# Performance work log

Hardware: AMD Instinct MI355X
Metric: run time of the kernel (lower is better)

## Reference

```python
import jax, jax.numpy as jnp
import numpy as np

LEAKY_SLOPE = 0.2  # tf.nn.leaky_relu default alpha
L2_EPS = 1e-12     # tf.nn.l2_normalize default epsilon


def setup_inputs() -> dict:
    key = jax.random.key(0)
    N, d, E, k = 100000, 64, 1600000, 3
    k0, k1, k2, k3 = jax.random.split(key, 4)
    x = jax.random.normal(k0, (N, d), dtype=jnp.float32)
    edge_index = jax.random.randint(k1, (2, E), 0, N, dtype=jnp.int32)
    scale = 1.0 / np.sqrt(d).astype(np.float32)
    W_gcn = jax.random.normal(k2, (k, d, d), dtype=jnp.float32) * scale
    W_int = jax.random.normal(k3, (k, d, d), dtype=jnp.float32) * scale
    b_gcn = jnp.zeros((k, d), dtype=jnp.float32)
    b_int = jnp.zeros((k, d), dtype=jnp.float32)
    return {"x": x, "edge_index": edge_index, "W_gcn": W_gcn, "b_gcn": b_gcn,
            "W_int": W_int, "b_int": b_int}


def _l2norm(h):
    sq = jnp.sum(h * h, axis=-1, keepdims=True)
    return h * jax.lax.rsqrt(jnp.maximum(sq, L2_EPS))


def reference(x, edge_index, W_gcn, b_gcn, W_int, b_int):
    N = x.shape[0]
    row, col = edge_index[0], edge_index[1]
    # LightGCN.norm_adj: symmetric normalization D^-1/2 A D^-1/2 (no self-loops)
    deg = jax.ops.segment_sum(jnp.ones_like(row, dtype=x.dtype), row, num_segments=N)
    dinv = jnp.where(deg > 0, jax.lax.rsqrt(deg), 0.0)
    w = dinv[row] * dinv[col]  # [E]

    def agg(h):
        # sparse normed_adj @ h : gather source feats, scale, scatter-add to dst
        return jax.ops.segment_sum(w[:, None] * h[col], row, num_segments=N)

    lrelu = lambda z: jax.nn.leaky_relu(z, LEAKY_SLOPE)
    h = x
    outs = [x]
    for i in range(W_gcn.shape[0]):
        ha = agg(h)  # [N, d]
        h = lrelu(ha @ W_gcn[i] + b_gcn[i]) + lrelu((h * ha) @ W_int[i] + b_int[i])
        outs.append(_l2norm(h))
    return jnp.concatenate(outs, axis=-1)  # [N, (k+1)*d]
```

## Files before the change

kernel.cpp:

```cpp
#include <hip/hip_runtime.h>


#define LEAKY 0.2f
#define NBK_MAX 512
#define TILE_A 4096
#define BCAP 5120

typedef unsigned short ushort_t;
typedef unsigned char uchar_t;
typedef short short8 __attribute__((ext_vector_type(8)));
typedef float f32x4 __attribute__((ext_vector_type(4)));
typedef float f32x2 __attribute__((ext_vector_type(2)));

__device__ __forceinline__ float lrelu(float z) { return z > 0.f ? z : LEAKY * z; }

__device__ __forceinline__ unsigned f2bf(float f) {
  unsigned u = __float_as_uint(f);
  return (u + 0x7FFFu + ((u >> 16) & 1u)) >> 16;
}

__device__ __forceinline__ float bf2f(unsigned u) {
  return __uint_as_float(u << 16);
}

__device__ __forceinline__ unsigned f2fp8(float f) {
  return (unsigned)__builtin_amdgcn_cvt_pk_fp8_f32(f, f, 0, false) & 0xFFu;
}

__device__ __forceinline__ int rfl(const int* p) {
  return __builtin_amdgcn_readfirstlane(*p);
}

__global__ __launch_bounds__(256) void bucket_k(const int* __restrict__ row,
                                                const int* __restrict__ col,
                                                int* __restrict__ tails,
                                                unsigned int* __restrict__ buckets,
                                                int E, int nbk) {
  __shared__ int bcnt[NBK_MAX], bex[NBK_MAX], bnext[NBK_MAX], gbase[NBK_MAX];
  __shared__ int ssc[256];
  int t = threadIdx.x;
  int ts = blockIdx.x * TILE_A;
  int tn = E - ts;
  if (tn > TILE_A) tn = TILE_A;
  bcnt[t] = 0;
  bcnt[t + 256] = 0;
  __syncthreads();
  for (int i = t; i < tn; i += 256) atomicAdd(&bcnt[row[ts + i] >> 8], 1);
  __syncthreads();
  int a0 = bcnt[2 * t], a1 = bcnt[2 * t + 1];
  ssc[t] = a0 + a1;
  __syncthreads();
  #pragma unroll
  for (int off = 1; off < 256; off <<= 1) {
    int x = (t >= off) ? ssc[t - off] : 0;
    __syncthreads();
    ssc[t] += x;
    __syncthreads();
  }
  int ex = ssc[t] - (a0 + a1);
  bex[2 * t] = ex;
  bex[2 * t + 1] = ex + a0;
  bnext[2 * t] = ex;
  bnext[2 * t + 1] = ex + a0;
  if (t < nbk && bcnt[t] > 0) gbase[t] = atomicAdd(&tails[t], bcnt[t]);
  int t2 = t + 256;
  if (t2 < nbk && bcnt[t2] > 0) gbase[t2] = atomicAdd(&tails[t2], bcnt[t2]);
  __syncthreads();
  for (int i = t; i < tn; i += 256) {
    int r = row[ts + i], c = col[ts + i];
    int b = r >> 8;
    int k = atomicAdd(&bnext[b], 1) - bex[b];
    int pos = gbase[b] + k;
    if (pos < BCAP)
      buckets[(size_t)b * BCAP + pos] = ((unsigned)(r & 255) << 24) | (unsigned)c;
  }
}

__global__ __launch_bounds__(512) void bkscan_k(const int* __restrict__ tails,
                                                int* __restrict__ bkbase,
                                                int* __restrict__ rp,
                                                int nbk, int N, int E) {
  __shared__ int s[512];
  int t = threadIdx.x;
  int v = (t < nbk) ? tails[t] : 0;
  s[t] = v;
  __syncthreads();
  #pragma unroll
  for (int off = 1; off < 512; off <<= 1) {
    int x = (t >= off) ? s[t - off] : 0;
    __syncthreads();
    s[t] += x;
    __syncthreads();
  }
  if (t < nbk) bkbase[t] = s[t] - v;
  if (t == 0) rp[N] = E;
}

__global__ __launch_bounds__(256) void csr_k(const int* __restrict__ tails,
                                             const int* __restrict__ bkbase,
                                             const unsigned int* __restrict__ buckets,
                                             int* __restrict__ rp,
                                             float* __restrict__ dinv,
                                             int* __restrict__ packed, int N) {
  __shared__ int cnt[256], sc[256], cnt2[256];
  int b = blockIdx.x, t = threadIdx.x;
  int row0 = b << 8;
  int nrows = N - row0;
  if (nrows > 256) nrows = 256;
  int cb = tails[b];
  if (cb > BCAP) cb = BCAP;
  int base = bkbase[b];
  const unsigned int* ent = buckets + (size_t)b * BCAP;
  cnt[t] = 0;
  __syncthreads();
  for (int i = t; i < cb; i += 256) atomicAdd(&cnt[ent[i] >> 24], 1);
  __syncthreads();
  int v = cnt[t];
  sc[t] = v;
  __syncthreads();
  #pragma unroll
  for (int off = 1; off < 256; off <<= 1) {
    int x = (t >= off) ? sc[t - off] : 0;
    __syncthreads();
    sc[t] += x;
    __syncthreads();
  }
  int ex = sc[t] - v;
  if (t < nrows) {
    rp[row0 + t] = base + ex;
    dinv[row0 + t] = (v > 0) ? rsqrtf((float)v) : 0.f;
  }
  cnt[t] = ex;
  cnt2[t] = 0;
  __syncthreads();
  for (int i = t; i < cb; i += 256) {
    unsigned e = ent[i];
    int rl = e >> 24;
    int slot = atomicAdd(&cnt2[rl], 1);
    packed[base + cnt[rl] + slot] = (int)(e & 0xFFFFFFu);
  }
}

__global__ __launch_bounds__(256) void copyx_k(const float* __restrict__ x,
                                               const float* __restrict__ dinv,
                                               float* __restrict__ out,
                                               ushort_t* __restrict__ xb,
                                               uchar_t* __restrict__ xg,
                                               int N, int ostride4) {
  int total = N * 16;
  int stride = gridDim.x * blockDim.x;
  for (int i = blockIdx.x * blockDim.x + threadIdx.x; i < total; i += stride) {
    int n = i >> 4, c4 = i & 15;
    float4 v = ((const float4*)x)[i];
    ((float4*)out)[(size_t)n * ostride4 + c4] = v;
    unsigned p0 = f2bf(v.x) | (f2bf(v.y) << 16);
    unsigned p1 = f2bf(v.z) | (f2bf(v.w) << 16);
    ((uint2*)xb)[i] = make_uint2(p0, p1);
    float dv = dinv[n];
    unsigned pkA =
        (unsigned)__builtin_amdgcn_cvt_pk_fp8_f32(v.x * dv, v.y * dv, 0, false);
    unsigned pkB =
        (unsigned)__builtin_amdgcn_cvt_pk_fp8_f32(v.z * dv, v.w * dv, 0, false);
    ((unsigned*)xg)[i] = (pkA & 0xFFFFu) | ((pkB & 0xFFFFu) << 16);
  }
}

__global__ __launch_bounds__(256) void packw_k(const float* __restrict__ Wg,
                                               const float* __restrict__ Wi,
                                               ushort_t* __restrict__ Wfrag,
                                               int total,
                                               int* __restrict__ tails, int nbk) {
  int tid = blockIdx.x * 256 + threadIdx.x;
  if (tid < nbk) tails[tid] = 0;
  if (tid >= total) return;
  int lane = tid & 63;
  int kh = (tid >> 6) & 1;
  int nt = (tid >> 7) & 3;
  int gm = (tid >> 9) & 1;
  int ly = tid >> 10;
  const float* W = (gm ? Wi : Wg) + (size_t)ly * 4096;
  int kb = (kh << 5) + ((lane >> 4) << 3);
  int n = (nt << 4) + (lane & 15);
  unsigned u[4];
  #pragma unroll
  for (int j = 0; j < 4; ++j) {
    unsigned lo = f2bf(W[(kb + 2 * j) * 64 + n]);
    unsigned hi = f2bf(W[(kb + 2 * j + 1) * 64 + n]);
    u[j] = lo | (hi << 16);
  }
  ((uint4*)Wfrag)[tid] = make_uint4(u[0], u[1], u[2], u[3]);
}

__global__ __launch_bounds__(256) void agg_k(const int* __restrict__ rp,
                                             const int* __restrict__ packed,
                                             const float* __restrict__ dinv,
                                             const uchar_t* __restrict__ gin,
                                             ushort_t* __restrict__ ha, int N) {
  int wv = (((blockIdx.x << 2) + (threadIdx.x >> 6)) << 1);
  if (wv >= N) return;
  int lane = threadIdx.x & 63;
  int grp = lane >> 3;
  int l8 = lane & 7;
  bool have1 = (wv + 1) < N;
  int s0 = rfl(&rp[wv]);
  int e0 = rfl(&rp[wv + 1]);
  int s1 = have1 ? rfl(&rp[wv + 1]) : 0;
  int e1 = have1 ? rfl(&rp[wv + 2]) : 0;
  float dr0 = __int_as_float(__builtin_amdgcn_readfirstlane(__float_as_int(dinv[wv])));
  float dr1 = have1 ? __int_as_float(__builtin_amdgcn_readfirstlane(
                          __float_as_int(dinv[wv + 1])))
                    : 0.f;
  float a0[8], a1[8];
  #pragma unroll
  for (int i = 0; i < 8; ++i) { a0[i] = 0.f; a1[i] = 0.f; }
  int bidx0 = grp << 2;
  int ch0 = s0, ch1 = s1;
  while (ch0 < e0 || ch1 < e1) {
    int m0 = e0 - ch0;
    if (m0 > 64) m0 = 64;
    int m1 = e1 - ch1;
    if (m1 > 64) m1 = 64;
    int cl0 = (m0 > 0 && lane < m0) ? packed[ch0 + lane] : 0;
    int cl1 = (m1 > 0 && lane < m1) ? packed[ch1 + lane] : 0;
    int mm = m0 > m1 ? m0 : m1;
    int nit = (mm + 7) >> 3;
    #pragma unroll 2
    for (int j = 0; j < nit; ++j) {
      int bi = bidx0 + (j << 5);
      int c0 = __builtin_amdgcn_ds_bpermute(bi, cl0);
      int c1 = __builtin_amdgcn_ds_bpermute(bi, cl1);
      int eidx = (j << 3) + grp;
      float msk0 = (eidx < m0) ? 1.f : 0.f;
      float msk1 = (eidx < m1) ? 1.f : 0.f;
      uint2 v0 = ((const uint2*)(gin + ((size_t)c0 << 6)))[l8];
      uint2 v1 = ((const uint2*)(gin + ((size_t)c1 << 6)))[l8];
      f32x2 d;
      d = __builtin_amdgcn_cvt_pk_f32_fp8((int)v0.x, false);
      a0[0] = fmaf(msk0, d[0], a0[0]);  a0[1] = fmaf(msk0, d[1], a0[1]);
      d = __builtin_amdgcn_cvt_pk_f32_fp8((int)v0.x, true);
      a0[2] = fmaf(msk0, d[0], a0[2]);  a0[3] = fmaf(msk0, d[1], a0[3]);
      d = __builtin_amdgcn_cvt_pk_f32_fp8((int)v0.y, false);
      a0[4] = fmaf(msk0, d[0], a0[4]);  a0[5] = fmaf(msk0, d[1], a0[5]);
      d = __builtin_amdgcn_cvt_pk_f32_fp8((int)v0.y, true);
      a0[6] = fmaf(msk0, d[0], a0[6]);  a0[7] = fmaf(msk0, d[1], a0[7]);
      d = __builtin_amdgcn_cvt_pk_f32_fp8((int)v1.x, false);
      a1[0] = fmaf(msk1, d[0], a1[0]);  a1[1] = fmaf(msk1, d[1], a1[1]);
      d = __builtin_amdgcn_cvt_pk_f32_fp8((int)v1.x, true);
      a1[2] = fmaf(msk1, d[0], a1[2]);  a1[3] = fmaf(msk1, d[1], a1[3]);
      d = __builtin_amdgcn_cvt_pk_f32_fp8((int)v1.y, false);
      a1[4] = fmaf(msk1, d[0], a1[4]);  a1[5] = fmaf(msk1, d[1], a1[5]);
      d = __builtin_amdgcn_cvt_pk_f32_fp8((int)v1.y, true);
      a1[6] = fmaf(msk1, d[0], a1[6]);  a1[7] = fmaf(msk1, d[1], a1[7]);
    }
    ch0 += 64;
    ch1 += 64;
  }
  #pragma unroll
  for (int off = 8; off < 64; off <<= 1)
    #pragma unroll
    for (int i = 0; i < 8; ++i) {
      a0[i] += __shfl_xor(a0[i], off);
      a1[i] += __shfl_xor(a1[i], off);
    }
  if (grp == 0) {
    unsigned u0 = f2bf(a0[0] * dr0) | (f2bf(a0[1] * dr0) << 16);
    unsigned u1 = f2bf(a0[2] * dr0) | (f2bf(a0[3] * dr0) << 16);
    unsigned u2 = f2bf(a0[4] * dr0) | (f2bf(a0[5] * dr0) << 16);
    unsigned u3 = f2bf(a0[6] * dr0) | (f2bf(a0[7] * dr0) << 16);
    ((uint4*)(ha + ((size_t)wv << 6)))[l8] = make_uint4(u0, u1, u2, u3);
  } else if (grp == 1 && have1) {
    unsigned u0 = f2bf(a1[0] * dr1) | (f2bf(a1[1] * dr1) << 16);
    unsigned u1 = f2bf(a1[2] * dr1) | (f2bf(a1[3] * dr1) << 16);
    unsigned u2 = f2bf(a1[4] * dr1) | (f2bf(a1[5] * dr1) << 16);
    unsigned u3 = f2bf(a1[6] * dr1) | (f2bf(a1[7] * dr1) << 16);
    ((uint4*)(ha + ((size_t)(wv + 1) << 6)))[l8] = make_uint4(u0, u1, u2, u3);
  }
}

__global__ __launch_bounds__(256) void gemmM_k(const ushort_t* __restrict__ ha,
                                               const ushort_t* __restrict__ hin,
                                               const ushort_t* __restrict__ Wfrag,
                                               const float* __restrict__ bg,
                                               const float* __restrict__ bi,
                                               const float* __restrict__ dinv,
                                               ushort_t* __restrict__ hout,
                                               uchar_t* __restrict__ gout,
                                               float* __restrict__ outp,
                                               int N, int ntiles, int ostride,
                                               int writeg) {
  int lane = threadIdx.x & 63;
  int gq = lane >> 4, ln15 = lane & 15;
  const short8* wf = (const short8*)Wfrag;
  short8 bG[8], bI[8];
  #pragma unroll
  for (int nt = 0; nt < 4; ++nt)
    #pragma unroll
    for (int kh = 0; kh < 2; ++kh) {
      bG[nt * 2 + kh] = wf[nt * 128 + kh * 64 + lane];
      bI[nt * 2 + kh] = wf[512 + nt * 128 + kh * 64 + lane];
    }
  float bgv[4], biv[4];
  #pragma unroll
  for (int nt = 0; nt < 4; ++nt) {
    bgv[nt] = bg[nt * 16 + ln15];
    biv[nt] = bi[nt * 16 + ln15];
  }
  int wid = (blockIdx.x << 2) + (threadIdx.x >> 6);
  int nw = gridDim.x << 2;
  for (int tile = wid; tile < ntiles; tile += nw) {
    int node0 = tile << 4;
    const short8* pa =
        (const short8*)(ha + (size_t)(node0 + ln15) * 64 + gq * 8);
    const short8* ph =
        (const short8*)(hin + (size_t)(node0 + ln15) * 64 + gq * 8);
    f32x4 acc1[4], acc2[4];
    #pragma unroll
    for (int nt = 0; nt < 4; ++nt) {
      acc1[nt] = (f32x4){bgv[nt], bgv[nt], bgv[nt], bgv[nt]};
      acc2[nt] = (f32x4){biv[nt], biv[nt], biv[nt], biv[nt]};
    }
    #pragma unroll
    for (int kh = 0; kh < 2; ++kh) {
      short8 af = pa[kh * 4];
      short8 hf = ph[kh * 4];
      short8 vmf;
      #pragma unroll
      for (int e2 = 0; e2 < 8; ++e2) {
        float fa = bf2f((ushort_t)af[e2]);
        float fh = bf2f((ushort_t)hf[e2]);
        vmf[e2] = (short)f2bf(fa * fh);
      }
      #pragma unroll
      for (int nt = 0; nt < 4; ++nt) {
        acc1[nt] = __builtin_amdgcn_mfma_f32_16x16x32_bf16(af, bG[nt * 2 + kh],
                                                           acc1[nt], 0, 0, 0);
        acc2[nt] = __builtin_amdgcn_mfma_f32_16x16x32_bf16(vmf, bI[nt * 2 + kh],
                                                           acc2[nt], 0, 0, 0);
      }
    }
    float z[4][4];
    float ssr[4] = {0.f, 0.f, 0.f, 0.f};
    #pragma unroll
    for (int nt = 0; nt < 4; ++nt)
      #pragma unroll
      for (int reg = 0; reg < 4; ++reg) {
        float zz = lrelu(acc1[nt][reg]) + lrelu(acc2[nt][reg]);
        z[nt][reg] = zz;
        ssr[reg] = fmaf(zz, zz, ssr[reg]);
      }
    #pragma unroll
    for (int off = 1; off < 16; off <<= 1)
      #pragma unroll
      for (int reg = 0; reg < 4; ++reg) ssr[reg] += __shfl_xor(ssr[reg], off);
    float inv[4];
    #pragma unroll
    for (int reg = 0; reg < 4; ++reg)
      inv[reg] = rsqrtf(fmaxf(ssr[reg], 1e-12f));
    #pragma unroll
    for (int reg = 0; reg < 4; ++reg) {
      int r = node0 + 4 * gq + reg;
      if (r < N) {
        float dv = dinv[r];
        #pragma unroll
        for (int nt = 0; nt < 4; ++nt) {
          outp[(size_t)r * ostride + nt * 16 + ln15] = z[nt][reg] * inv[reg];
          hout[(size_t)r * 64 + nt * 16 + ln15] = (ushort_t)f2bf(z[nt][reg]);
          if (writeg)
            gout[(size_t)r * 64 + nt * 16 + ln15] =
                (uchar_t)f2fp8(z[nt][reg] * dv);
        }
      }
    }
  }
}

extern "C" void kernel_launch(void* const* d_in, const int* in_sizes, int n_in,
                              void* d_out, int out_size, void* d_ws, size_t ws_size,
                              hipStream_t stream) {
  const float* x  = (const float*)d_in[0];
  const int*   ei = (const int*)d_in[1];
  const float* Wg = (const float*)d_in[2];
  const float* bg = (const float*)d_in[3];
  const float* Wi = (const float*)d_in[4];
  const float* bi = (const float*)d_in[5];
  float* out = (float*)d_out;

  const int d = 64;
  const int N = in_sizes[0] / d;
  const int E = in_sizes[1] / 2;
  const int K = in_sizes[2] / (d * d);
  const int* row = ei;
  const int* col = ei + E;
  const int nbk = (N + 255) / 256;
  const int N16 = (N + 15) & ~15;
  const int ntiles = N16 / 16;
  const int ostride = (K + 1) * d;

  char* ws = (char*)d_ws;
  size_t off = 0;
  auto alloc = [&](size_t bytes) {
    char* p = ws + off;
    off = (off + bytes + 255) & ~(size_t)255;
    return p;
  };
  int*   tails  = (int*)alloc((size_t)NBK_MAX * 4);
  int*   bkbase = (int*)alloc((size_t)NBK_MAX * 4);
  int*   rp     = (int*)alloc((size_t)(N + 1) * 4);
  float* dinv   = (float*)alloc((size_t)N16 * 4);
  unsigned int* buckets = (unsigned int*)alloc((size_t)nbk * BCAP * 4);
  int*   packed = (int*)alloc((size_t)E * 4);
  ushort_t* ha  = (ushort_t*)alloc((size_t)N16 * d * 2);
  ushort_t* hb0 = (ushort_t*)alloc((size_t)N16 * d * 2);
  ushort_t* hb1 = (ushort_t*)alloc((size_t)N16 * d * 2);
  ushort_t* xb  = (ushort_t*)alloc((size_t)N16 * d * 2);
  uchar_t* hg0  = (uchar_t*)alloc((size_t)N16 * d);
  uchar_t* hg1  = (uchar_t*)alloc((size_t)N16 * d);
  uchar_t* xg   = (uchar_t*)alloc((size_t)N16 * d);
  ushort_t* Wfrag = (ushort_t*)alloc((size_t)K * 8192 * 2);
  (void)ws_size;

  int wtotal = K * 1024;
  packw_k<<<(wtotal + 255) / 256, 256, 0, stream>>>(Wg, Wi, Wfrag, wtotal,
                                                    tails, nbk);
  int ntA = (E + TILE_A - 1) / TILE_A;
  bucket_k<<<ntA, 256, 0, stream>>>(row, col, tails, buckets, E, nbk);
  bkscan_k<<<1, 512, 0, stream>>>(tails, bkbase, rp, nbk, N, E);
  csr_k<<<nbk, 256, 0, stream>>>(tails, bkbase, buckets, rp, dinv, packed, N);
  copyx_k<<<2048, 256, 0, stream>>>(x, dinv, out, xb, xg, N, ostride / 4);

  const ushort_t* hin = xb;
  const uchar_t* gin = xg;
  ushort_t* hbufs[2] = {hb0, hb1};
  uchar_t* gbufs[2] = {hg0, hg1};
  int aggblocks = (N + 7) / 8;
  for (int i = 0; i < K; ++i) {
    ushort_t* hout = hbufs[i & 1];
    uchar_t* gout = gbufs[i & 1];
    agg_k<<<aggblocks, 256, 0, stream>>>(rp, packed, dinv, gin, ha, N);
    gemmM_k<<<1024, 256, 0, stream>>>(
        ha, hin, Wfrag + (size_t)i * 8192, bg + (size_t)i * d,
        bi + (size_t)i * d, dinv, hout, gout, out + (size_t)(i + 1) * d,
        N, ntiles, ostride, (i + 1 < K) ? 1 : 0);
    hin = hout;
    gin = gout;
  }
}
```

Measured before the change: 223.7 us.

## Fuse CSR preprocessing kernels and aggregate four rows per wavefront

The bucket-scan kernel is folded into bucket_k through a last-block-done atomic counter, and the x copy/convert kernel is folded into csr_k using per-block shared dinv. This removes two launches and a dependent global dinv read. agg_k now handles four destination rows per wavefront instead of two, giving more independent gathers in flight at the cost of extra registers. The last layer's gemm also skips writing the bf16 and fp8 hidden buffers it never reads. The last-block pattern depends on atomics for memory visibility.

New measurement: 236.5 us. 5.8% more time.

```diff
diff --git a/kernel.cpp b/kernel.cpp
--- a/kernel.cpp
+++ b/kernel.cpp
@@ -31,138 +31,8 @@
   return __builtin_amdgcn_readfirstlane(*p);
 }
 
-__global__ __launch_bounds__(256) void bucket_k(const int* __restrict__ row,
-                                                const int* __restrict__ col,
-                                                int* __restrict__ tails,
-                                                unsigned int* __restrict__ buckets,
-                                                int E, int nbk) {
-  __shared__ int bcnt[NBK_MAX], bex[NBK_MAX], bnext[NBK_MAX], gbase[NBK_MAX];
-  __shared__ int ssc[256];
-  int t = threadIdx.x;
-  int ts = blockIdx.x * TILE_A;
-  int tn = E - ts;
-  if (tn > TILE_A) tn = TILE_A;
-  bcnt[t] = 0;
-  bcnt[t + 256] = 0;
-  __syncthreads();
-  for (int i = t; i < tn; i += 256) atomicAdd(&bcnt[row[ts + i] >> 8], 1);
-  __syncthreads();
-  int a0 = bcnt[2 * t], a1 = bcnt[2 * t + 1];
-  ssc[t] = a0 + a1;
-  __syncthreads();
-  #pragma unroll
-  for (int off = 1; off < 256; off <<= 1) {
-    int x = (t >= off) ? ssc[t - off] : 0;
-    __syncthreads();
-    ssc[t] += x;
-    __syncthreads();
-  }
-  int ex = ssc[t] - (a0 + a1);
-  bex[2 * t] = ex;
-  bex[2 * t + 1] = ex + a0;
-  bnext[2 * t] = ex;
-  bnext[2 * t + 1] = ex + a0;
-  if (t < nbk && bcnt[t] > 0) gbase[t] = atomicAdd(&tails[t], bcnt[t]);
-  int t2 = t + 256;
-  if (t2 < nbk && bcnt[t2] > 0) gbase[t2] = atomicAdd(&tails[t2], bcnt[t2]);
-  __syncthreads();
-  for (int i = t; i < tn; i += 256) {
-    int r = row[ts + i], c = col[ts + i];
-    int b = r >> 8;
-    int k = atomicAdd(&bnext[b], 1) - bex[b];
-    int pos = gbase[b] + k;
-    if (pos < BCAP)
-      buckets[(size_t)b * BCAP + pos] = ((unsigned)(r & 255) << 24) | (unsigned)c;
-  }
-}
-
-__global__ __launch_bounds__(512) void bkscan_k(const int* __restrict__ tails,
-                                                int* __restrict__ bkbase,
-                                                int* __restrict__ rp,
-                                                int nbk, int N, int E) {
-  __shared__ int s[512];
-  int t = threadIdx.x;
-  int v = (t < nbk) ? tails[t] : 0;
-  s[t] = v;
-  __syncthreads();
-  #pragma unroll
-  for (int off = 1; off < 512; off <<= 1) {
-    int x = (t >= off) ? s[t - off] : 0;
-    __syncthreads();
-    s[t] += x;
-    __syncthreads();
-  }
-  if (t < nbk) bkbase[t] = s[t] - v;
-  if (t == 0) rp[N] = E;
-}
-
-__global__ __launch_bounds__(256) void csr_k(const int* __restrict__ tails,
-                                             const int* __restrict__ bkbase,
-                                             const unsigned int* __restrict__ buckets,
-                                             int* __restrict__ rp,
-                                             float* __restrict__ dinv,
-                                             int* __restrict__ packed, int N) {
-  __shared__ int cnt[256], sc[256], cnt2[256];
-  int b = blockIdx.x, t = threadIdx.x;
-  int row0 = b << 8;
-  int nrows = N - row0;
-  if (nrows > 256) nrows = 256;
-  int cb = tails[b];
-  if (cb > BCAP) cb = BCAP;
-  int base = bkbase[b];
-  const unsigned int* ent = buckets + (size_t)b * BCAP;
-  cnt[t] = 0;
-  __syncthreads();
-  for (int i = t; i < cb; i += 256) atomicAdd(&cnt[ent[i] >> 24], 1);
-  __syncthreads();
-  int v = cnt[t];
-  sc[t] = v;
-  __syncthreads();
-  #pragma unroll
-  for (int off = 1; off < 256; off <<= 1) {
-    int x = (t >= off) ? sc[t - off] : 0;
-    __syncthreads();
-    sc[t] += x;
-    __syncthreads();
-  }
-  int ex = sc[t] - v;
-  if (t < nrows) {
-    rp[row0 + t] = base + ex;
-    dinv[row0 + t] = (v > 0) ? rsqrtf((float)v) : 0.f;
-  }
-  cnt[t] = ex;
-  cnt2[t] = 0;
-  __syncthreads();
-  for (int i = t; i < cb; i += 256) {
-    unsigned e = ent[i];
-    int rl = e >> 24;
-    int slot = atomicAdd(&cnt2[rl], 1);
-    packed[base + cnt[rl] + slot] = (int)(e & 0xFFFFFFu);
-  }
-}
-
-__global__ __launch_bounds__(256) void copyx_k(const float* __restrict__ x,
-                                               const float* __restrict__ dinv,
-                                               float* __restrict__ out,
-                                               ushort_t* __restrict__ xb,
-                                               uchar_t* __restrict__ xg,
-                                               int N, int ostride4) {
-  int total = N * 16;
-  int stride = gridDim.x * blockDim.x;
-  for (int i = blockIdx.x * blockDim.x + threadIdx.x; i < total; i += stride) {
-    int n = i >> 4, c4 = i & 15;
-    float4 v = ((const float4*)x)[i];
-    ((float4*)out)[(size_t)n * ostride4 + c4] = v;
-    unsigned p0 = f2bf(v.x) | (f2bf(v.y) << 16);
-    unsigned p1 = f2bf(v.z) | (f2bf(v.w) << 16);
-    ((uint2*)xb)[i] = make_uint2(p0, p1);
-    float dv = dinv[n];
-    unsigned pkA =
-        (unsigned)__builtin_amdgcn_cvt_pk_fp8_f32(v.x * dv, v.y * dv, 0, false);
-    unsigned pkB =
-        (unsigned)__builtin_amdgcn_cvt_pk_fp8_f32(v.z * dv, v.w * dv, 0, false);
-    ((unsigned*)xg)[i] = (pkA & 0xFFFFu) | ((pkB & 0xFFFFu) << 16);
-  }
+__device__ __forceinline__ float rflf(const float* p) {
+  return __int_as_float(__builtin_amdgcn_readfirstlane(__float_as_int(*p)));
 }
 
 __global__ __launch_bounds__(256) void packw_k(const float* __restrict__ Wg,
@@ -171,7 +41,7 @@
                                                int total,
                                                int* __restrict__ tails, int nbk) {
   int tid = blockIdx.x * 256 + threadIdx.x;
-  if (tid < nbk) tails[tid] = 0;
+  if (tid <= nbk) tails[tid] = 0;
   if (tid >= total) return;
   int lane = tid & 63;
   int kh = (tid >> 6) & 1;
@@ -191,69 +61,233 @@
   ((uint4*)Wfrag)[tid] = make_uint4(u[0], u[1], u[2], u[3]);
 }
 
+__global__ __launch_bounds__(256) void bucket_k(const int* __restrict__ row,
+                                                const int* __restrict__ col,
+                                                int* __restrict__ tails,
+                                                unsigned int* __restrict__ buckets,
+                                                int* __restrict__ bkbase,
+                                                int* __restrict__ rp,
+                                                int E, int nbk, int N) {
+  __shared__ int bcnt[NBK_MAX], bex[NBK_MAX], bnext[NBK_MAX], gbase[NBK_MAX];
+  __shared__ int ssc[256];
+  __shared__ int amLast;
+  int t = threadIdx.x;
+  int ts = blockIdx.x * TILE_A;
+  int tn = E - ts;
+  if (tn > TILE_A) tn = TILE_A;
+  bcnt[t] = 0;
+  bcnt[t + 256] = 0;
+  __syncthreads();
+  for (int i = t; i < tn; i += 256) atomicAdd(&bcnt[row[ts + i] >> 8], 1);
+  __syncthreads();
+  int a0 = bcnt[2 * t], a1 = bcnt[2 * t + 1];
+  ssc[t] = a0 + a1;
+  __syncthreads();
+  #pragma unroll
+  for (int off = 1; off < 256; off <<= 1) {
+    int x = (t >= off) ? ssc[t - off] : 0;
+    __syncthreads();
+    ssc[t] += x;
+    __syncthreads();
+  }
+  int ex = ssc[t] - (a0 + a1);
+  bex[2 * t] = ex;
+  bex[2 * t + 1] = ex + a0;
+  bnext[2 * t] = ex;
+  bnext[2 * t + 1] = ex + a0;
+  if (t < nbk && bcnt[t] > 0) gbase[t] = atomicAdd(&tails[t], bcnt[t]);
+  int t2 = t + 256;
+  if (t2 < nbk && bcnt[t2] > 0) gbase[t2] = atomicAdd(&tails[t2], bcnt[t2]);
+  __syncthreads();
+  for (int i = t; i < tn; i += 256) {
+    int r = row[ts + i], c = col[ts + i];
+    int b = r >> 8;
+    int k = atomicAdd(&bnext[b], 1) - bex[b];
+    int pos = gbase[b] + k;
+    if (pos < BCAP)
+      buckets[(size_t)b * BCAP + pos] = ((unsigned)(r & 255) << 24) | (unsigned)c;
+  }
+  __syncthreads();
+  if (t == 0) amLast = (atomicAdd(&tails[nbk], 1) == (int)gridDim.x - 1);
+  __syncthreads();
+  if (amLast) {
+    int i0 = 2 * t, i1 = 2 * t + 1;
+    int v0 = (i0 < nbk) ? atomicAdd(&tails[i0], 0) : 0;
+    int v1 = (i1 < nbk) ? atomicAdd(&tails[i1], 0) : 0;
+    ssc[t] = v0 + v1;
+    __syncthreads();
+    #pragma unroll
+    for (int off = 1; off < 256; off <<= 1) {
+      int x = (t >= off) ? ssc[t - off] : 0;
+      __syncthreads();
+      ssc[t] += x;
+      __syncthreads();
+    }
+    int ex2 = ssc[t] - (v0 + v1);
+    if (i0 < nbk) bkbase[i0] = ex2;
+    if (i1 < nbk) bkbase[i1] = ex2 + v0;
+    if (t == 0) rp[N] = E;
+  }
+}
+
+__global__ __launch_bounds__(256) void csr_k(const int* __restrict__ tails,
+                                             const int* __restrict__ bkbase,
+                                             const unsigned int* __restrict__ buckets,
+                                             int* __restrict__ rp,
+                                             float* __restrict__ dinv,
+                                             int* __restrict__ packed,
+                                             const float* __restrict__ x,
+                                             float* __restrict__ out,
+                                             ushort_t* __restrict__ xb,
+                                             uchar_t* __restrict__ xg,
+                                             int N, int ostride4) {
+  __shared__ int cnt[256], sc[256], cnt2[256];
+  __shared__ float sdinv[256];
+  int b = blockIdx.x, t = threadIdx.x;
+  int row0 = b << 8;
+  int nrows = N - row0;
+  if (nrows > 256) nrows = 256;
+  int cb = tails[b];
+  if (cb > BCAP) cb = BCAP;
+  int base = bkbase[b];
+  const unsigned int* ent = buckets + (size_t)b * BCAP;
+  cnt[t] = 0;
+  __syncthreads();
+  for (int i = t; i < cb; i += 256) atomicAdd(&cnt[ent[i] >> 24], 1);
+  __syncthreads();
+  int v = cnt[t];
+  sc[t] = v;
+  __syncthreads();
+  #pragma unroll
+  for (int off = 1; off < 256; off <<= 1) {
+    int x2 = (t >= off) ? sc[t - off] : 0;
+    __syncthreads();
+    sc[t] += x2;
+    __syncthreads();
+  }
+  int ex = sc[t] - v;
+  float dvv = (v > 0) ? rsqrtf((float)v) : 0.f;
+  sdinv[t] = dvv;
+  if (t < nrows) {
+    rp[row0 + t] = base + ex;
+    dinv[row0 + t] = dvv;
+  }
+  cnt[t] = ex;
+  cnt2[t] = 0;
+  __syncthreads();
+  for (int i = t; i < cb; i += 256) {
+    unsigned e = ent[i];
+    int rl = e >> 24;
+    int slot = atomicAdd(&cnt2[rl], 1);
+    packed[base + cnt[rl] + slot] = (int)(e & 0xFFFFFFu);
+  }
+  int base4 = row0 << 4;
+  int tot4 = nrows << 4;
+  for (int i = t; i < tot4; i += 256) {
+    int rl = i >> 4, c4 = i & 15;
+    float4 vx = ((const float4*)x)[base4 + i];
+    ((float4*)out)[(size_t)(row0 + rl) * ostride4 + c4] = vx;
+    unsigned p0 = f2bf(vx.x) | (f2bf(vx.y) << 16);
+    unsigned p1 = f2bf(vx.z) | (f2bf(vx.w) << 16);
+    ((uint2*)xb)[base4 + i] = make_uint2(p0, p1);
+    float dv = sdinv[rl];
+    unsigned pkA =
+        (unsigned)__builtin_amdgcn_cvt_pk_fp8_f32(vx.x * dv, vx.y * dv, 0, false);
+    unsigned pkB =
+        (unsigned)__builtin_amdgcn_cvt_pk_fp8_f32(vx.z * dv, vx.w * dv, 0, false);
+    ((unsigned*)xg)[base4 + i] = (pkA & 0xFFFFu) | ((pkB & 0xFFFFu) << 16);
+  }
+}
+
 __global__ __launch_bounds__(256) void agg_k(const int* __restrict__ rp,
                                              const int* __restrict__ packed,
                                              const float* __restrict__ dinv,
                                              const uchar_t* __restrict__ gin,
                                              ushort_t* __restrict__ ha, int N) {
-  int wv = (((blockIdx.x << 2) + (threadIdx.x >> 6)) << 1);
+  int wv = (((blockIdx.x << 2) + (threadIdx.x >> 6)) << 2);
   if (wv >= N) return;
   int lane = threadIdx.x & 63;
   int grp = lane >> 3;
   int l8 = lane & 7;
-  bool have1 = (wv + 1) < N;
+  bool h1 = (wv + 1) < N, h2 = (wv + 2) < N, h3 = (wv + 3) < N;
   int s0 = rfl(&rp[wv]);
   int e0 = rfl(&rp[wv + 1]);
-  int s1 = have1 ? rfl(&rp[wv + 1]) : 0;
-  int e1 = have1 ? rfl(&rp[wv + 2]) : 0;
-  float dr0 = __int_as_float(__builtin_amdgcn_readfirstlane(__float_as_int(dinv[wv])));
-  float dr1 = have1 ? __int_as_float(__builtin_amdgcn_readfirstlane(
-                          __float_as_int(dinv[wv + 1])))
-                    : 0.f;
-  float a0[8], a1[8];
-  #pragma unroll
-  for (int i = 0; i < 8; ++i) { a0[i] = 0.f; a1[i] = 0.f; }
+  int s1 = h1 ? rfl(&rp[wv + 1]) : 0, e1 = h1 ? rfl(&rp[wv + 2]) : 0;
+  int s2 = h2 ? rfl(&rp[wv + 2]) : 0, e2 = h2 ? rfl(&rp[wv + 3]) : 0;
+  int s3 = h3 ? rfl(&rp[wv + 3]) : 0, e3 = h3 ? rfl(&rp[wv + 4]) : 0;
+  float dr0 = rflf(&dinv[wv]);
+  float dr1 = h1 ? rflf(&dinv[wv + 1]) : 0.f;
+  float dr2 = h2 ? rflf(&dinv[wv + 2]) : 0.f;
+  float dr3 = h3 ? rflf(&dinv[wv + 3]) : 0.f;
+  float a0[8], a1[8], a2[8], a3[8];
+  #pragma unroll
+  for (int i = 0; i < 8; ++i) { a0[i] = 0.f; a1[i] = 0.f; a2[i] = 0.f; a3[i] = 0.f; }
   int bidx0 = grp << 2;
-  int ch0 = s0, ch1 = s1;
-  while (ch0 < e0 || ch1 < e1) {
-    int m0 = e0 - ch0;
-    if (m0 > 64) m0 = 64;
-    int m1 = e1 - ch1;
-    if (m1 > 64) m1 = 64;
+  int ch0 = s0, ch1 = s1, ch2 = s2, ch3 = s3;
+  while (ch0 < e0 || ch1 < e1 || ch2 < e2 || ch3 < e3) {
+    int m0 = e0 - ch0; if (m0 > 64) m0 = 64;
+    int m1 = e1 - ch1; if (m1 > 64) m1 = 64;
+    int m2 = e2 - ch2; if (m2 > 64) m2 = 64;
+    int m3 = e3 - ch3; if (m3 > 64) m3 = 64;
     int cl0 = (m0 > 0 && lane < m0) ? packed[ch0 + lane] : 0;
     int cl1 = (m1 > 0 && lane < m1) ? packed[ch1 + lane] : 0;
+    int cl2 = (m2 > 0 && lane < m2) ? packed[ch2 + lane] : 0;
+    int cl3 = (m3 > 0 && lane < m3) ? packed[ch3 + lane] : 0;
     int mm = m0 > m1 ? m0 : m1;
+    if (m2 > mm) mm = m2;
+    if (m3 > mm) mm = m3;
     int nit = (mm + 7) >> 3;
     #pragma unroll 2
     for (int j = 0; j < nit; ++j) {
       int bi = bidx0 + (j << 5);
       int c0 = __builtin_amdgcn_ds_bpermute(bi, cl0);
       int c1 = __builtin_amdgcn_ds_bpermute(bi, cl1);
+      int c2 = __builtin_amdgcn_ds_bpermute(bi, cl2);
+      int c3 = __builtin_amdgcn_ds_bpermute(bi, cl3);
       int eidx = (j << 3) + grp;
-      float msk0 = (eidx < m0) ? 1.f : 0.f;
-      float msk1 = (eidx < m1) ? 1.f : 0.f;
+      float k0 = (eidx < m0) ? 1.f : 0.f;
+      float k1 = (eidx < m1) ? 1.f : 0.f;
+      float k2 = (eidx < m2) ? 1.f : 0.f;
+      float k3 = (eidx < m3) ? 1.f : 0.f;
       uint2 v0 = ((const uint2*)(gin + ((size_t)c0 << 6)))[l8];
       uint2 v1 = ((const uint2*)(gin + ((size_t)c1 << 6)))[l8];
+      uint2 v2 = ((const uint2*)(gin + ((size_t)c2 << 6)))[l8];
+      uint2 v3 = ((const uint2*)(gin + ((size_t)c3 << 6)))[l8];
       f32x2 d;
       d = __builtin_amdgcn_cvt_pk_f32_fp8((int)v0.x, false);
-      a0[0] = fmaf(msk0, d[0], a0[0]);  a0[1] = fmaf(msk0, d[1], a0[1]);
+      a0[0] = fmaf(k0, d[0], a0[0]);  a0[1] = fmaf(k0, d[1], a0[1]);
       d = __builtin_amdgcn_cvt_pk_f32_fp8((int)v0.x, true);
-      a0[2] = fmaf(msk0, d[0], a0[2]);  a0[3] = fmaf(msk0, d[1], a0[3]);
+      a0[2] = fmaf(k0, d[0], a0[2]);  a0[3] = fmaf(k0, d[1], a0[3]);
       d = __builtin_amdgcn_cvt_pk_f32_fp8((int)v0.y, false);
-      a0[4] = fmaf(msk0, d[0], a0[4]);  a0[5] = fmaf(msk0, d[1], a0[5]);
+      a0[4] = fmaf(k0, d[0], a0[4]);  a0[5] = fmaf(k0, d[1], a0[5]);
       d = __builtin_amdgcn_cvt_pk_f32_fp8((int)v0.y, true);
-      a0[6] = fmaf(msk0, d[0], a0[6]);  a0[7] = fmaf(msk0, d[1], a0[7]);
+      a0[6] = fmaf(k0, d[0], a0[6]);  a0[7] = fmaf(k0, d[1], a0[7]);
       d = __builtin_amdgcn_cvt_pk_f32_fp8((int)v1.x, false);
-      a1[0] = fmaf(msk1, d[0], a1[0]);  a1[1] = fmaf(msk1, d[1], a1[1]);
+      a1[0] = fmaf(k1, d[0], a1[0]);  a1[1] = fmaf(k1, d[1], a1[1]);
       d = __builtin_amdgcn_cvt_pk_f32_fp8((int)v1.x, true);
-      a1[2] = fmaf(msk1, d[0], a1[2]);  a1[3] = fmaf(msk1, d[1], a1[3]);
+      a1[2] = fmaf(k1, d[0], a1[2]);  a1[3] = fmaf(k1, d[1], a1[3]);
       d = __builtin_amdgcn_cvt_pk_f32_fp8((int)v1.y, false);
-      a1[4] = fmaf(msk1, d[0], a1[4]);  a1[5] = fmaf(msk1, d[1], a1[5]);
+      a1[4] = fmaf(k1, d[0], a1[4]);  a1[5] = fmaf(k1, d[1], a1[5]);
       d = __builtin_amdgcn_cvt_pk_f32_fp8((int)v1.y, true);
-      a1[6] = fmaf(msk1, d[0], a1[6]);  a1[7] = fmaf(msk1, d[1], a1[7]);
-    }
-    ch0 += 64;
-    ch1 += 64;
+      a1[6] = fmaf(k1, d[0], a1[6]);  a1[7] = fmaf(k1, d[1], a1[7]);
+      d = __builtin_amdgcn_cvt_pk_f32_fp8((int)v2.x, false);
+      a2[0] = fmaf(k2, d[0], a2[0]);  a2[1] = fmaf(k2, d[1], a2[1]);
+      d = __builtin_amdgcn_cvt_pk_f32_fp8((int)v2.x, true);
+      a2[2] = fmaf(k2, d[0], a2[2]);  a2[3] = fmaf(k2, d[1], a2[3]);
+      d = __builtin_amdgcn_cvt_pk_f32_fp8((int)v2.y, false);
+      a2[4] = fmaf(k2, d[0], a2[4]);  a2[5] = fmaf(k2, d[1], a2[5]);
+      d = __builtin_amdgcn_cvt_pk_f32_fp8((int)v2.y, true);
+      a2[6] = fmaf(k2, d[0], a2[6]);  a2[7] = fmaf(k2, d[1], a2[7]);
+      d = __builtin_amdgcn_cvt_pk_f32_fp8((int)v3.x, false);
+      a3[0] = fmaf(k3, d[0], a3[0]);  a3[1] = fmaf(k3, d[1], a3[1]);
+      d = __builtin_amdgcn_cvt_pk_f32_fp8((int)v3.x, true);
+      a3[2] = fmaf(k3, d[0], a3[2]);  a3[3] = fmaf(k3, d[1], a3[3]);
+      d = __builtin_amdgcn_cvt_pk_f32_fp8((int)v3.y, false);
+      a3[4] = fmaf(k3, d[0], a3[4]);  a3[5] = fmaf(k3, d[1], a3[5]);
+      d = __builtin_amdgcn_cvt_pk_f32_fp8((int)v3.y, true);
+      a3[6] = fmaf(k3, d[0], a3[6]);  a3[7] = fmaf(k3, d[1], a3[7]);
+    }
+    ch0 += 64; ch1 += 64; ch2 += 64; ch3 += 64;
   }
   #pragma unroll
   for (int off = 8; off < 64; off <<= 1)
@@ -261,6 +295,8 @@
     for (int i = 0; i < 8; ++i) {
       a0[i] += __shfl_xor(a0[i], off);
       a1[i] += __shfl_xor(a1[i], off);
+      a2[i] += __shfl_xor(a2[i], off);
+      a3[i] += __shfl_xor(a3[i], off);
     }
   if (grp == 0) {
     unsigned u0 = f2bf(a0[0] * dr0) | (f2bf(a0[1] * dr0) << 16);
@@ -268,12 +304,24 @@
     unsigned u2 = f2bf(a0[4] * dr0) | (f2bf(a0[5] * dr0) << 16);
     unsigned u3 = f2bf(a0[6] * dr0) | (f2bf(a0[7] * dr0) << 16);
     ((uint4*)(ha + ((size_t)wv << 6)))[l8] = make_uint4(u0, u1, u2, u3);
-  } else if (grp == 1 && have1) {
+  } else if (grp == 1 && h1) {
     unsigned u0 = f2bf(a1[0] * dr1) | (f2bf(a1[1] * dr1) << 16);
     unsigned u1 = f2bf(a1[2] * dr1) | (f2bf(a1[3] * dr1) << 16);
     unsigned u2 = f2bf(a1[4] * dr1) | (f2bf(a1[5] * dr1) << 16);
     unsigned u3 = f2bf(a1[6] * dr1) | (f2bf(a1[7] * dr1) << 16);
     ((uint4*)(ha + ((size_t)(wv + 1) << 6)))[l8] = make_uint4(u0, u1, u2, u3);
+  } else if (grp == 2 && h2) {
+    unsigned u0 = f2bf(a2[0] * dr2) | (f2bf(a2[1] * dr2) << 16);
+    unsigned u1 = f2bf(a2[2] * dr2) | (f2bf(a2[3] * dr2) << 16);
+    unsigned u2 = f2bf(a2[4] * dr2) | (f2bf(a2[5] * dr2) << 16);
+    unsigned u3 = f2bf(a2[6] * dr2) | (f2bf(a2[7] * dr2) << 16);
+    ((uint4*)(ha + ((size_t)(wv + 2) << 6)))[l8] = make_uint4(u0, u1, u2, u3);
+  } else if (grp == 3 && h3) {
+    unsigned u0 = f2bf(a3[0] * dr3) | (f2bf(a3[1] * dr3) << 16);
+    unsigned u1 = f2bf(a3[2] * dr3) | (f2bf(a3[3] * dr3) << 16);
+    unsigned u2 = f2bf(a3[4] * dr3) | (f2bf(a3[5] * dr3) << 16);
+    unsigned u3 = f2bf(a3[6] * dr3) | (f2bf(a3[7] * dr3) << 16);
+    ((uint4*)(ha + ((size_t)(wv + 3) << 6)))[l8] = make_uint4(u0, u1, u2, u3);
   }
 }
 
@@ -287,7 +335,7 @@
                                                uchar_t* __restrict__ gout,
                                                float* __restrict__ outp,
                                                int N, int ntiles, int ostride,
-                                               int writeg) {
+                                               int writehg) {
   int lane = threadIdx.x & 63;
   int gq = lane >> 4, ln15 = lane & 15;
   const short8* wf = (const short8*)Wfrag;
@@ -364,10 +412,11 @@
         #pragma unroll
         for (int nt = 0; nt < 4; ++nt) {
           outp[(size_t)r * ostride + nt * 16 + ln15] = z[nt][reg] * inv[reg];
-          hout[(size_t)r * 64 + nt * 16 + ln15] = (ushort_t)f2bf(z[nt][reg]);
-          if (writeg)
+          if (writehg) {
+            hout[(size_t)r * 64 + nt * 16 + ln15] = (ushort_t)f2bf(z[nt][reg]);
             gout[(size_t)r * 64 + nt * 16 + ln15] =
                 (uchar_t)f2fp8(z[nt][reg] * dv);
+          }
         }
       }
     }
@@ -403,7 +452,7 @@
     off = (off + bytes + 255) & ~(size_t)255;
     return p;
   };
-  int*   tails  = (int*)alloc((size_t)NBK_MAX * 4);
+  int*   tails  = (int*)alloc((size_t)(NBK_MAX + 1) * 4);
   int*   bkbase = (int*)alloc((size_t)NBK_MAX * 4);
   int*   rp     = (int*)alloc((size_t)(N + 1) * 4);
   float* dinv   = (float*)alloc((size_t)N16 * 4);
@@ -423,16 +472,16 @@
   packw_k<<<(wtotal + 255) / 256, 256, 0, stream>>>(Wg, Wi, Wfrag, wtotal,
                                                     tails, nbk);
   int ntA = (E + TILE_A - 1) / TILE_A;
-  bucket_k<<<ntA, 256, 0, stream>>>(row, col, tails, buckets, E, nbk);
-  bkscan_k<<<1, 512, 0, stream>>>(tails, bkbase, rp, nbk, N, E);
-  csr_k<<<nbk, 256, 0, stream>>>(tails, bkbase, buckets, rp, dinv, packed, N);
-  copyx_k<<<2048, 256, 0, stream>>>(x, dinv, out, xb, xg, N, ostride / 4);
+  bucket_k<<<ntA, 256, 0, stream>>>(row, col, tails, buckets, bkbase, rp,
+                                    E, nbk, N);
+  csr_k<<<nbk, 256, 0, stream>>>(tails, bkbase, buckets, rp, dinv, packed,
+                                 x, out, xb, xg, N, ostride / 4);
 
   const ushort_t* hin = xb;
   const uchar_t* gin = xg;
   ushort_t* hbufs[2] = {hb0, hb1};
   uchar_t* gbufs[2] = {hg0, hg1};
-  int aggblocks = (N + 7) / 8;
+  int aggblocks = (N + 15) / 16;
   for (int i = 0; i < K; ++i) {
     ushort_t* hout = hbufs[i & 1];
     uchar_t* gout = gbufs[i & 1];
```
